# Kernel tuning notes

Hardware: AMD Instinct MI355X
Metric: run time of the kernel (lower is better)

## Reference

```python
import jax, jax.numpy as jnp
import numpy as np
import math

D = 1024      # hidden_size
H = 16        # num_heads
HD = D // H   # head_dim = 64
ROPE = 64     # rope_dim == head_dim (full-head rotation, empty pass-through)
E = 8         # num_experts
F = 2560
BASE = 10000.0
EPS = 1e-5
SPECIALS = jnp.arange(2, 8)  # special_tokens indices {2..7} used as global tokens


def _ln(x, w, b):
    m = x.mean(-1, keepdims=True)
    v = x.var(-1, keepdims=True)  # biased var, matches torch LayerNorm
    return (x - m) / jnp.sqrt(v + EPS) * w + b


def _rope(x, cos, sin):
    # x: [B,H,T,HD]; rotate first ROPE dims via half-split (NOT rotate-half interleave)
    x1, x2 = x[..., : ROPE // 2], x[..., ROPE // 2 : ROPE]
    rot = jnp.concatenate([x1 * cos - x2 * sin, x1 * sin + x2 * cos], axis=-1)
    return jnp.concatenate([rot, x[..., ROPE:]], axis=-1)


def setup_inputs() -> dict:
    key = jax.random.key(0)
    ks = jax.random.split(key, 8)
    B, T = 1, 1024
    g = lambda k, shape, s: (jax.random.normal(k, shape, jnp.float32) * s)
    return {
        "x": g(ks[0], (B, T, D), 1.0),
        "input_ids": jax.random.randint(ks[1], (B, T), 0, 32000),
        "ln1_w": jnp.ones((D,), jnp.float32), "ln1_b": jnp.zeros((D,), jnp.float32),
        "qkv_w": g(ks[2], (D, 3 * D), 0.02), "qkv_b": jnp.zeros((3 * D,), jnp.float32),
        "attn_out_w": g(ks[3], (D, D), 0.02), "attn_out_b": jnp.zeros((D,), jnp.float32),
        "ln2_w": jnp.ones((D,), jnp.float32), "ln2_b": jnp.zeros((D,), jnp.float32),
        "gate_w": g(ks[4], (D, E), 0.02), "gate_b": jnp.zeros((E,), jnp.float32),
        "fc_w": g(ks[5], (E, D, 2 * F), 0.02), "fc_b": jnp.zeros((E, 2 * F), jnp.float32),
        "eout_w": g(ks[6], (E, F, D), 0.02), "eout_b": jnp.zeros((E, D), jnp.float32),
    }


def _block(x, input_ids, ln1_w, ln1_b, qkv_w, qkv_b, attn_out_w, attn_out_b,
           ln2_w, ln2_b, gate_w, gate_b, fc_w, fc_b, eout_w, eout_b):
    B, T, _ = x.shape
    # --- self-attention (pre-norm) ---
    h = _ln(x, ln1_w, ln1_b)
    qkv = h @ qkv_w + qkv_b
    q, k, v = jnp.split(qkv, 3, axis=-1)
    resh = lambda t: t.reshape(B, T, H, HD).transpose(0, 2, 1, 3)  # [B,H,T,HD]
    q, k, v = resh(q), resh(k), resh(v)
    pos = jnp.arange(T, dtype=jnp.float32)
    inv = 1.0 / (BASE ** (jnp.arange(0, ROPE, 2, dtype=jnp.float32) / ROPE))
    fr = pos[:, None] * inv[None, :]            # [T, ROPE/2]
    cos, sin = jnp.cos(fr), jnp.sin(fr)
    q = _rope(q, cos, sin)
    k = _rope(k, cos, sin)
    causal = jnp.tril(jnp.ones((T, T), bool))
    glob = (input_ids[..., None] == SPECIALS).any(-1)            # [B,T]
    allowed = causal[None, None] | glob[:, None, :, None]        # [B,1,T,T]
    logits = jnp.einsum('bhqd,bhkd->bhqk', q, k) / math.sqrt(HD)
    neg = -jnp.finfo(logits.dtype).max
    logits = jnp.where(allowed, logits, neg)
    aw = jax.nn.softmax(logits, axis=-1)
    attn = jnp.einsum('bhqk,bhkd->bhqd', aw, v).transpose(0, 2, 1, 3).reshape(B, T, H * HD)
    x = x + (attn @ attn_out_w + attn_out_b)
    # --- MoE GEGLU FFN (hard top-1 routing) ---
    h2 = _ln(x, ln2_w, ln2_b)
    gp = jax.nn.softmax(h2 @ gate_w + gate_b, axis=-1)           # [B,T,E]
    gw = gp.max(-1)
    gi = gp.argmax(-1)
    xf = h2.reshape(-1, D)
    gif = gi.reshape(-1)
    gwf = gw.reshape(-1)
    N = xf.shape[0]
    outf = jnp.zeros((N, D), x.dtype)
    for e in range(E):  # fixed small expert loop; select by routing mask
        h12 = xf @ fc_w[e] + fc_b[e]
        x1, x2 = h12[:, :F], h12[:, F:]
        y = (x1 * jax.nn.gelu(x2, approximate=False)) @ eout_w[e] + eout_b[e]
        outf = outf + jnp.where((gif == e)[:, None], y, 0.0)
    outf = outf * gwf[:, None]
    sums = jax.ops.segment_sum(gwf, gif, num_segments=E)
    counts = jax.ops.segment_sum(jnp.ones_like(gwf), gif, num_segments=E)
    usage = sums / (counts + 1e-8)
    moe_loss = jnp.sum((usage - 1.0 / E) ** 2)
    return x + outf.reshape(B, T, D), moe_loss


def reference(x, input_ids, ln1_w, ln1_b, qkv_w, qkv_b, attn_out_w, attn_out_b,
              ln2_w, ln2_b, gate_w, gate_b, fc_w, fc_b, eout_w, eout_b):
    return _block(x, input_ids, ln1_w, ln1_b, qkv_w, qkv_b, attn_out_w, attn_out_b,
                  ln2_w, ln2_b, gate_w, gate_b, fc_w, fc_b, eout_w, eout_b)
```

## Files before the change

kernel.cpp:

```cpp
#include <hip/hip_runtime.h>
#include <float.h>
#include <math.h>
#include <stdint.h>

#define T_ 1024
#define D_ 1024
#define H_ 16
#define HD_ 64
#define E_ 8
#define F_ 2560
#define D3_ 3072
#define F2_ 5120

#define WS_H    0u
#define WS_QKV  1048576u
#define WS_ATTN 4194304u
#define WS_X2   5242880u
#define WS_H2   6291456u
#define WS_A    7340032u
#define WS_GW   9961472u
#define WS_GI   9962496u
#define WS_OFFS 9963520u
#define WS_PERM 9963536u

typedef short short8 __attribute__((ext_vector_type(8)));
typedef short short4v __attribute__((ext_vector_type(4)));
typedef __bf16 bf16x8 __attribute__((ext_vector_type(8)));
typedef float floatx4 __attribute__((ext_vector_type(4)));

union FragU { short8 s; bf16x8 b; };

__device__ __forceinline__ short f2bf(float f) {
    union { float f; uint32_t u; } a; a.f = f;
    uint32_t r = a.u + 0x7fffu + ((a.u >> 16) & 1u);
    return (short)(r >> 16);
}

__device__ __forceinline__ void cvt16(const float4& a0, const float4& a1,
                                      const float4& a2, const float4& a3,
                                      short8& c0, short8& c1) {
    c0[0]=f2bf(a0.x); c0[1]=f2bf(a0.y); c0[2]=f2bf(a0.z); c0[3]=f2bf(a0.w);
    c0[4]=f2bf(a1.x); c0[5]=f2bf(a1.y); c0[6]=f2bf(a1.z); c0[7]=f2bf(a1.w);
    c1[0]=f2bf(a2.x); c1[1]=f2bf(a2.y); c1[2]=f2bf(a2.z); c1[3]=f2bf(a2.w);
    c1[4]=f2bf(a3.x); c1[5]=f2bf(a3.y); c1[6]=f2bf(a3.z); c1[7]=f2bf(a3.w);
}

#define GEMM_IDS \
    const int tid  = threadIdx.x;                 \
    const int a_m  = tid >> 1;                    \
    const int a_kh = (tid & 1) * 16;              \
    const int lane = tid & 63, wave = tid >> 6;   \
    const int wm = wave & 1,  wn = wave >> 1;     \
    const int quad = lane >> 4, lm = lane & 15;

__global__ __launch_bounds__(256) void gemm_mfma_full(
    const float* __restrict__ A, int lda,
    const float* __restrict__ B, int ldb,
    const float* __restrict__ bias,
    float* __restrict__ C, int ldc, int K)
{
    __shared__ __align__(16) short As[4*128*8];
    __shared__ __align__(16) short Bs[64*40];
    const int row0 = blockIdx.y * 128, col0 = blockIdx.x * 64;
    GEMM_IDS
    const int b_n = tid >> 2, b_kc = tid & 3;
    floatx4 acc[4][2];
    #pragma unroll
    for (int i=0;i<4;i++)
        #pragma unroll
        for (int j=0;j<2;j++) acc[i][j] = (floatx4){0.f,0.f,0.f,0.f};

    const float* apx = A + (size_t)(row0 + a_m) * lda + a_kh;
    const float* bpx = B + (size_t)(b_kc*8) * ldb + col0 + b_n;
    const int kcA = (tid & 1) * 2;

    float4 a0, a1, a2, a3; float bvv[8];
    a0 = *(const float4*)(apx);     a1 = *(const float4*)(apx + 4);
    a2 = *(const float4*)(apx + 8); a3 = *(const float4*)(apx + 12);
    #pragma unroll
    for (int j=0;j<8;j++) bvv[j] = bpx[(size_t)j*ldb];

    for (int k0 = 0; k0 < K; k0 += 32) {
        __syncthreads();
        short8 c0, c1, cb;
        cvt16(a0,a1,a2,a3,c0,c1);
        #pragma unroll
        for (int j=0;j<8;j++) cb[j] = f2bf(bvv[j]);
        *(short8*)&As[((kcA  )*128 + a_m)*8] = c0;
        *(short8*)&As[((kcA+1)*128 + a_m)*8] = c1;
        *(short8*)&Bs[b_n*40 + b_kc*8] = cb;
        __syncthreads();
        if (k0 + 32 < K) {
            const float* ap2 = apx + k0 + 32;
            a0 = *(const float4*)(ap2);     a1 = *(const float4*)(ap2 + 4);
            a2 = *(const float4*)(ap2 + 8); a3 = *(const float4*)(ap2 + 12);
            const float* bp2 = bpx + (size_t)(k0+32) * ldb;
            #pragma unroll
            for (int j=0;j<8;j++) bvv[j] = bp2[(size_t)j*ldb];
        }
        FragU fa[4], fb[2];
        #pragma unroll
        for (int i=0;i<4;i++) fa[i].s = *(short8*)&As[(quad*128 + wm*64 + i*16 + lm)*8];
        #pragma unroll
        for (int j=0;j<2;j++) fb[j].s = *(short8*)&Bs[(wn*32 + j*16 + lm)*40 + quad*8];
        #pragma unroll
        for (int i=0;i<4;i++)
            #pragma unroll
            for (int j=0;j<2;j++)
                acc[i][j] = __builtin_amdgcn_mfma_f32_16x16x32_bf16(fa[i].b, fb[j].b, acc[i][j], 0,0,0);
    }
    #pragma unroll
    for (int i=0;i<4;i++)
        #pragma unroll
        for (int j=0;j<2;j++) {
            int col = col0 + wn*32 + j*16 + lm;
            float bb = bias ? bias[col] : 0.f;
            #pragma unroll
            for (int r=0;r<4;r++) {
                int row = row0 + wm*64 + i*16 + quad*4 + r;
                C[(size_t)row*ldc + col] = acc[i][j][r] + bb;
            }
        }
}

__global__ __launch_bounds__(256) void gemm_mfma_acc(
    const float* __restrict__ A, int lda,
    const float* __restrict__ B, int ldb, long sB,
    const int* __restrict__ offs, const int* __restrict__ perm,
    float* __restrict__ Cacc, int ldc, int K, int nsk)
{
    const int sk = blockIdx.z % nsk;
    const int e  = blockIdx.z / nsk;
    int off = 0, Ne = T_;
    if (offs) { off = offs[e]; Ne = offs[e+1] - off; }
    const int row0 = blockIdx.y * 128;
    if (row0 >= Ne) return;
    const int col0 = blockIdx.x * 64;
    B += (long)e * sB;

    __shared__ __align__(16) short As[4*128*8];
    __shared__ __align__(16) short Bs[64*40];
    __shared__ int toks[128];
    GEMM_IDS
    const int b_n = tid >> 2, b_kc = tid & 3;
    if (tid < 128) {
        int r = row0 + tid;
        toks[tid] = offs ? ((r < Ne) ? perm[off + r] : -1) : r;
    }
    __syncthreads();

    floatx4 acc[4][2];
    #pragma unroll
    for (int i=0;i<4;i++)
        #pragma unroll
        for (int j=0;j<2;j++) acc[i][j] = (floatx4){0.f,0.f,0.f,0.f};

    const int tokA = toks[a_m];
    const float* apx = (tokA >= 0) ? (A + (size_t)tokA * lda + a_kh) : nullptr;
    const float* bpx = B + (size_t)(b_kc*8) * ldb + col0 + b_n;
    const int kcA = (tid & 1) * 2;
    const int Kp = K / nsk;
    const int koff = sk * Kp, kend = koff + Kp;

    float4 a0, a1, a2, a3; float bvv[8];
    a0 = make_float4(0,0,0,0); a1 = a0; a2 = a0; a3 = a0;
    if (apx) {
        a0 = *(const float4*)(apx + koff);     a1 = *(const float4*)(apx + koff + 4);
        a2 = *(const float4*)(apx + koff + 8); a3 = *(const float4*)(apx + koff + 12);
    }
    {
        const float* bp2 = bpx + (size_t)koff * ldb;
        #pragma unroll
        for (int j=0;j<8;j++) bvv[j] = bp2[(size_t)j*ldb];
    }

    for (int k0 = koff; k0 < kend; k0 += 32) {
        __syncthreads();
        short8 c0, c1, cb;
        cvt16(a0,a1,a2,a3,c0,c1);
        #pragma unroll
        for (int j=0;j<8;j++) cb[j] = f2bf(bvv[j]);
        *(short8*)&As[((kcA  )*128 + a_m)*8] = c0;
        *(short8*)&As[((kcA+1)*128 + a_m)*8] = c1;
        *(short8*)&Bs[b_n*40 + b_kc*8] = cb;
        __syncthreads();
        if (k0 + 32 < kend) {
            if (apx) {
                const float* ap2 = apx + k0 + 32;
                a0 = *(const float4*)(ap2);     a1 = *(const float4*)(ap2 + 4);
                a2 = *(const float4*)(ap2 + 8); a3 = *(const float4*)(ap2 + 12);
            }
            const float* bp2 = bpx + (size_t)(k0+32) * ldb;
            #pragma unroll
            for (int j=0;j<8;j++) bvv[j] = bp2[(size_t)j*ldb];
        }
        FragU fa[4], fb[2];
        #pragma unroll
        for (int i=0;i<4;i++) fa[i].s = *(short8*)&As[(quad*128 + wm*64 + i*16 + lm)*8];
        #pragma unroll
        for (int j=0;j<2;j++) fb[j].s = *(short8*)&Bs[(wn*32 + j*16 + lm)*40 + quad*8];
        #pragma unroll
        for (int i=0;i<4;i++)
            #pragma unroll
            for (int j=0;j<2;j++)
                acc[i][j] = __builtin_amdgcn_mfma_f32_16x16x32_bf16(fa[i].b, fb[j].b, acc[i][j], 0,0,0);
    }
    #pragma unroll
    for (int i=0;i<4;i++)
        #pragma unroll
        for (int j=0;j<2;j++) {
            int col = col0 + wn*32 + j*16 + lm;
            #pragma unroll
            for (int r=0;r<4;r++) {
                int tk = toks[wm*64 + i*16 + quad*4 + r];
                if (tk >= 0) atomicAdd(&Cacc[(size_t)tk*ldc + col], acc[i][j][r]);
            }
        }
}

__global__ __launch_bounds__(256) void moe_fc_mfma(
    const float* __restrict__ h2, const float* __restrict__ fcw,
    const float* __restrict__ fcb, const int* __restrict__ offs,
    const int* __restrict__ perm, float* __restrict__ aout)
{
    const int e = blockIdx.z;
    const int off = offs[e];
    const int Ne = offs[e+1] - off;
    const int row0 = blockIdx.y * 128;
    if (row0 >= Ne) return;
    const int col0 = blockIdx.x * 32;

    __shared__ __align__(16) short As[4*128*8];
    __shared__ __align__(16) short B1s[32*40];
    __shared__ __align__(16) short B2s[32*40];
    __shared__ int toks[128];
    GEMM_IDS
    const int n_l = tid & 31, kg = tid >> 5;
    if (tid < 128) {
        int r = row0 + tid;
        toks[tid] = (r < Ne) ? perm[off + r] : -1;
    }
    __syncthreads();

    floatx4 acc1[4], acc2[4];
    #pragma unroll
    for (int i=0;i<4;i++) {
        acc1[i] = (floatx4){0.f,0.f,0.f,0.f};
        acc2[i] = (floatx4){0.f,0.f,0.f,0.f};
    }

    const float* W = fcw + (size_t)e * D_ * F2_;
    const int tokA = toks[a_m];
    const float* apx = (tokA >= 0) ? (h2 + (size_t)tokA * D_ + a_kh) : nullptr;
    const float* bpx = W + (size_t)(kg*4) * F2_ + col0 + n_l;
    const int kcA = (tid & 1) * 2;

    float4 a0, a1, a2, a3; float b1v[4], b2v[4];
    a0 = make_float4(0,0,0,0); a1 = a0; a2 = a0; a3 = a0;
    if (apx) {
        a0 = *(const float4*)(apx);     a1 = *(const float4*)(apx + 4);
        a2 = *(const float4*)(apx + 8); a3 = *(const float4*)(apx + 12);
    }
    #pragma unroll
    for (int j=0;j<4;j++) { b1v[j] = bpx[(size_t)j*F2_]; b2v[j] = bpx[(size_t)j*F2_ + F_]; }

    for (int k0 = 0; k0 < D_; k0 += 32) {
        __syncthreads();
        short8 c0, c1;
        short4v cb1, cb2;
        cvt16(a0,a1,a2,a3,c0,c1);
        #pragma unroll
        for (int j=0;j<4;j++) { cb1[j] = f2bf(b1v[j]); cb2[j] = f2bf(b2v[j]); }
        *(short8*)&As[((kcA  )*128 + a_m)*8] = c0;
        *(short8*)&As[((kcA+1)*128 + a_m)*8] = c1;
        *(short4v*)&B1s[n_l*40 + kg*4] = cb1;
        *(short4v*)&B2s[n_l*40 + kg*4] = cb2;
        __syncthreads();
        if (k0 + 32 < D_) {
            if (apx) {
                const float* ap2 = apx + k0 + 32;
                a0 = *(const float4*)(ap2);     a1 = *(const float4*)(ap2 + 4);
                a2 = *(const float4*)(ap2 + 8); a3 = *(const float4*)(ap2 + 12);
            }
            const float* bp2 = bpx + (size_t)(k0+32) * F2_;
            #pragma unroll
            for (int j=0;j<4;j++) { b1v[j] = bp2[(size_t)j*F2_]; b2v[j] = bp2[(size_t)j*F2_ + F_]; }
        }
        FragU fa[4], fb1, fb2;
        #pragma unroll
        for (int i=0;i<4;i++) fa[i].s = *(short8*)&As[(quad*128 + wm*64 + i*16 + lm)*8];
        fb1.s = *(short8*)&B1s[(wn*16 + lm)*40 + quad*8];
        fb2.s = *(short8*)&B2s[(wn*16 + lm)*40 + quad*8];
        #pragma unroll
        for (int i=0;i<4;i++) {
            acc1[i] = __builtin_amdgcn_mfma_f32_16x16x32_bf16(fa[i].b, fb1.b, acc1[i], 0,0,0);
            acc2[i] = __builtin_amdgcn_mfma_f32_16x16x32_bf16(fa[i].b, fb2.b, acc2[i], 0,0,0);
        }
    }
    {
        int col = col0 + wn*16 + lm;
        float b1 = fcb[(size_t)e*F2_ + col];
        float b2 = fcb[(size_t)e*F2_ + F_ + col];
        #pragma unroll
        for (int i=0;i<4;i++)
            #pragma unroll
            for (int r=0;r<4;r++) {
                int tk = toks[wm*64 + i*16 + quad*4 + r];
                if (tk < 0) continue;
                float v1 = acc1[i][r] + b1;
                float v2 = acc2[i][r] + b2;
                float g = v2 * 0.5f * (1.0f + erff(v2 * 0.70710678118654752f));
                aout[(size_t)tk*F_ + col] = v1 * g;
            }
    }
}

__global__ __launch_bounds__(128) void flash_attn(
    const float* __restrict__ qkv, const int* __restrict__ ids,
    float* __restrict__ attnout)
{
    const int h  = blockIdx.y;
    const int q0 = blockIdx.x * 32;
    const int tid = threadIdx.x;
    const int lane = tid & 63, w = tid >> 6;
    const int quad = lane >> 4, lm = lane & 15;

    __shared__ __align__(16) short Qs[32*72];
    __shared__ __align__(16) short Ks[64*72];
    __shared__ __align__(16) short Vt[64*72];
    __shared__ __align__(16) short Ps[2][16*72];
    __shared__ int globf[32];

    {
        int row = tid >> 2, c = (tid & 3) * 16;
        const float* qp = qkv + (size_t)(q0 + row) * D3_ + h * HD_ + c;
        float4 f0 = *(const float4*)(qp);
        float4 f1 = *(const float4*)(qp + 4);
        float4 f2 = *(const float4*)(qp + 8);
        float4 f3 = *(const float4*)(qp + 12);
        short8 s0, s1;
        cvt16(f0, f1, f2, f3, s0, s1);
        *(short8*)&Qs[row*72 + c]     = s0;
        *(short8*)&Qs[row*72 + c + 8] = s1;
    }
    if (tid < 32) {
        int id = ids[q0 + tid];
        globf[tid] = (id >= 2 && id <= 7) ? 1 : 0;
    }
    __syncthreads();

    FragU QA[2];
    #pragma unroll
    for (int s = 0; s < 2; s++)
        QA[s].s = *(short8*)&Qs[(w*16 + lm)*72 + s*32 + quad*8];

    int any = 0;
    #pragma unroll
    for (int i = 0; i < 32; i++) any |= globf[i];
    const int nt = any ? (T_/64) : ((q0 + 31) >> 6) + 1;

    int gq[4]; int qidx[4];
    #pragma unroll
    for (int r = 0; r < 4; r++) {
        int ql = w*16 + quad*4 + r;
        qidx[r] = q0 + ql;
        gq[r] = globf[ql];
    }

    float mrow[4] = {-1e30f, -1e30f, -1e30f, -1e30f};
    float lrow[4] = {0.f, 0.f, 0.f, 0.f};
    floatx4 Oacc[4];
    #pragma unroll
    for (int n = 0; n < 4; n++) Oacc[n] = (floatx4){0.f, 0.f, 0.f, 0.f};

    for (int kt = 0; kt < nt; kt++) {
        __syncthreads();
        #pragma unroll
        for (int rep = 0; rep < 2; rep++) {
            int key = (tid >> 2) + rep*32;
            int c = (tid & 3) * 16;
            const float* kp = qkv + (size_t)(kt*64 + key) * D3_ + D_ + h*HD_ + c;
            float4 f0 = *(const float4*)(kp);
            float4 f1 = *(const float4*)(kp + 4);
            float4 f2 = *(const float4*)(kp + 8);
            float4 f3 = *(const float4*)(kp + 12);
            short8 s0, s1;
            cvt16(f0, f1, f2, f3, s0, s1);
            *(short8*)&Ks[key*72 + c]     = s0;
            *(short8*)&Ks[key*72 + c + 8] = s1;
        }
        #pragma unroll
        for (int rep = 0; rep < 8; rep++) {
            int lin = tid + rep*128;
            int key = lin >> 4;
            int c = (lin & 15) * 4;
            const float* vp = qkv + (size_t)(kt*64 + key) * D3_ + 2*D_ + h*HD_ + c;
            float4 f = *(const float4*)vp;
            Vt[(c+0)*72 + key] = f2bf(f.x);
            Vt[(c+1)*72 + key] = f2bf(f.y);
            Vt[(c+2)*72 + key] = f2bf(f.z);
            Vt[(c+3)*72 + key] = f2bf(f.w);
        }
        __syncthreads();

        floatx4 Sv[4];
        #pragma unroll
        for (int n = 0; n < 4; n++) {
            Sv[n] = (floatx4){0.f, 0.f, 0.f, 0.f};
            #pragma unroll
            for (int s = 0; s < 2; s++) {
                FragU KB;
                KB.s = *(short8*)&Ks[(n*16 + lm)*72 + s*32 + quad*8];
                Sv[n] = __builtin_amdgcn_mfma_f32_16x16x32_bf16(QA[s].b, KB.b, Sv[n], 0, 0, 0);
            }
        }
        #pragma unroll
        for (int n = 0; n < 4; n++) {
            int key = kt*64 + n*16 + lm;
            #pragma unroll
            for (int r = 0; r < 4; r++) {
                float v = Sv[n][r] * 0.125f;
                if (!gq[r] && key > qidx[r]) v = -1e30f;
                Sv[n][r] = v;
            }
        }
        float mnew[4], alpha[4], tsum[4];
        #pragma unroll
        for (int r = 0; r < 4; r++) {
            float tm = fmaxf(fmaxf(Sv[0][r], Sv[1][r]), fmaxf(Sv[2][r], Sv[3][r]));
            #pragma unroll
            for (int x = 1; x < 16; x <<= 1) tm = fmaxf(tm, __shfl_xor(tm, x));
            mnew[r] = fmaxf(mrow[r], tm);
            alpha[r] = __expf(mrow[r] - mnew[r]);
            mrow[r] = mnew[r];
            tsum[r] = 0.f;
        }
        #pragma unroll
        for (int n = 0; n < 4; n++) {
            #pragma unroll
            for (int r = 0; r < 4; r++) {
                float p = __expf(Sv[n][r] - mnew[r]);
                tsum[r] += p;
                Ps[w][(quad*4 + r)*72 + n*16 + lm] = f2bf(p);
            }
        }
        #pragma unroll
        for (int r = 0; r < 4; r++) {
            #pragma unroll
            for (int x = 1; x < 16; x <<= 1) tsum[r] += __shfl_xor(tsum[r], x);
            lrow[r] = lrow[r] * alpha[r] + tsum[r];
        }
        #pragma unroll
        for (int n = 0; n < 4; n++)
            #pragma unroll
            for (int r = 0; r < 4; r++) Oacc[n][r] *= alpha[r];

        #pragma unroll
        for (int s = 0; s < 2; s++) {
            FragU PA;
            PA.s = *(short8*)&Ps[w][lm*72 + s*32 + quad*8];
            #pragma unroll
            for (int n = 0; n < 4; n++) {
                FragU VB;
                VB.s = *(short8*)&Vt[(n*16 + lm)*72 + s*32 + quad*8];
                Oacc[n] = __builtin_amdgcn_mfma_f32_16x16x32_bf16(PA.b, VB.b, Oacc[n], 0, 0, 0);
            }
        }
    }

    #pragma unroll
    for (int n = 0; n < 4; n++)
        #pragma unroll
        for (int r = 0; r < 4; r++) {
            float o = Oacc[n][r] / lrow[r];
            attnout[(size_t)qidx[r]*D_ + h*HD_ + n*16 + lm] = o;
        }
}

__global__ __launch_bounds__(256) void ep_attn(
    const float* __restrict__ x, const float* __restrict__ sacc,
    const float* __restrict__ aob, float* __restrict__ x2)
{
    int row = blockIdx.x, tid = threadIdx.x;
    float4 xv = ((const float4*)(x + (size_t)row*D_))[tid];
    float4 sv = ((const float4*)(sacc + (size_t)row*D_))[tid];
    float4 bv = ((const float4*)aob)[tid];
    float4 o;
    o.x = xv.x + sv.x + bv.x; o.y = xv.y + sv.y + bv.y;
    o.z = xv.z + sv.z + bv.z; o.w = xv.w + sv.w + bv.w;
    ((float4*)(x2 + (size_t)row*D_))[tid] = o;
}

__global__ __launch_bounds__(256) void ep_moe(
    const float* __restrict__ x2, const float* __restrict__ sacc,
    const float* __restrict__ eob, const float* __restrict__ gw,
    const int* __restrict__ gi, float* __restrict__ out)
{
    int row = blockIdx.x, tid = threadIdx.x;
    float g = gw[row];
    int e = gi[row];
    float4 xv = ((const float4*)(x2 + (size_t)row*D_))[tid];
    float4 sv = ((const float4*)(sacc + (size_t)row*D_))[tid];
    float4 bv = ((const float4*)(eob + (size_t)e*D_))[tid];
    float4 o;
    o.x = xv.x + g*(sv.x + bv.x); o.y = xv.y + g*(sv.y + bv.y);
    o.z = xv.z + g*(sv.z + bv.z); o.w = xv.w + g*(sv.w + bv.w);
    ((float4*)(out + (size_t)row*D_))[tid] = o;
}

__global__ __launch_bounds__(256) void ln_kernel(
    const float* __restrict__ x, const float* __restrict__ w,
    const float* __restrict__ b, float* __restrict__ out)
{
    const int row = blockIdx.x, tid = threadIdx.x;
    const int lane = tid & 63, wave = tid >> 6;
    float4 v = ((const float4*)(x + (size_t)row * D_))[tid];
    float s  = v.x + v.y + v.z + v.w;
    float sq = v.x*v.x + v.y*v.y + v.z*v.z + v.w*v.w;
    #pragma unroll
    for (int off = 32; off; off >>= 1) {
        s  += __shfl_down(s, off);
        sq += __shfl_down(sq, off);
    }
    __shared__ float rs[4], rq[4], mv[2];
    if (lane == 0) { rs[wave] = s; rq[wave] = sq; }
    __syncthreads();
    if (tid == 0) {
        float ts = rs[0]+rs[1]+rs[2]+rs[3];
        float tq = rq[0]+rq[1]+rq[2]+rq[3];
        float mean = ts * (1.0f / D_);
        float var  = tq * (1.0f / D_) - mean*mean;
        mv[0] = mean; mv[1] = rsqrtf(var + 1e-5f);
    }
    __syncthreads();
    float mean = mv[0], rstd = mv[1];
    float4 wv = ((const float4*)w)[tid];
    float4 bv = ((const float4*)b)[tid];
    float4 o;
    o.x = (v.x-mean)*rstd*wv.x + bv.x;
    o.y = (v.y-mean)*rstd*wv.y + bv.y;
    o.z = (v.z-mean)*rstd*wv.z + bv.z;
    o.w = (v.w-mean)*rstd*wv.w + bv.w;
    ((float4*)(out + (size_t)row * D_))[tid] = o;
}

__global__ __launch_bounds__(256) void rope_kernel(float* __restrict__ qkv)
{
    int gid = blockIdx.x * 256 + threadIdx.x;
    int t = gid >> 9;
    int r = gid & 511;
    int h = r >> 5;
    int d = r & 31;
    float inv = exp2f((float)d * -0.4152410118609203f);
    float fr = (float)t * inv;
    float s, c;
    sincosf(fr, &s, &c);
    float* base = qkv + (size_t)t*D3_ + h*HD_ + d;
    float q1 = base[0], q2 = base[32];
    base[0]  = q1*c - q2*s;
    base[32] = q1*s + q2*c;
    float* kb = base + D_;
    float k1 = kb[0], k2 = kb[32];
    kb[0]  = k1*c - k2*s;
    kb[32] = k1*s + k2*c;
}

__global__ __launch_bounds__(256) void ln2_gate_kernel(
    const float* __restrict__ x2, const float* __restrict__ w,
    const float* __restrict__ b, const float* __restrict__ gwm,
    const float* __restrict__ gbv, float* __restrict__ h2,
    int* __restrict__ gi, float* __restrict__ gw)
{
    const int row = blockIdx.x, tid = threadIdx.x;
    const int lane = tid & 63, wave = tid >> 6;
    float4 v = ((const float4*)(x2 + (size_t)row * D_))[tid];
    float s  = v.x + v.y + v.z + v.w;
    float sq = v.x*v.x + v.y*v.y + v.z*v.z + v.w*v.w;
    #pragma unroll
    for (int off = 32; off; off >>= 1) {
        s  += __shfl_down(s, off);
        sq += __shfl_down(sq, off);
    }
    __shared__ float rs[4], rq[4], mv[2];
    if (lane == 0) { rs[wave] = s; rq[wave] = sq; }
    __syncthreads();
    if (tid == 0) {
        float ts = rs[0]+rs[1]+rs[2]+rs[3];
        float tq = rq[0]+rq[1]+rq[2]+rq[3];
        float mean = ts * (1.0f / D_);
        float var  = tq * (1.0f / D_) - mean*mean;
        mv[0] = mean; mv[1] = rsqrtf(var + 1e-5f);
    }
    __syncthreads();
    float mean = mv[0], rstd = mv[1];
    float4 wv = ((const float4*)w)[tid];
    float4 bv = ((const float4*)b)[tid];
    float hv[4];
    hv[0] = (v.x-mean)*rstd*wv.x + bv.x;
    hv[1] = (v.y-mean)*rstd*wv.y + bv.y;
    hv[2] = (v.z-mean)*rstd*wv.z + bv.z;
    hv[3] = (v.w-mean)*rstd*wv.w + bv.w;
    float4 o; o.x=hv[0]; o.y=hv[1]; o.z=hv[2]; o.w=hv[3];
    ((float4*)(h2 + (size_t)row * D_))[tid] = o;

    float acc[E_] = {};
    int c = tid * 4;
    #pragma unroll
    for (int j = 0; j < 4; j++) {
        const float* gr = gwm + (size_t)(c+j) * E_;
        #pragma unroll
        for (int e = 0; e < E_; e++) acc[e] += hv[j] * gr[e];
    }
    #pragma unroll
    for (int off = 32; off; off >>= 1)
        #pragma unroll
        for (int e = 0; e < E_; e++) acc[e] += __shfl_down(acc[e], off);
    __shared__ float gred[4][E_];
    if (lane == 0)
        for (int e = 0; e < E_; e++) gred[wave][e] = acc[e];
    __syncthreads();
    if (tid == 0) {
        float lg[E_];
        float mxl = -FLT_MAX; int mi = 0;
        for (int e = 0; e < E_; e++)
            lg[e] = gred[0][e]+gred[1][e]+gred[2][e]+gred[3][e] + gbv[e];
        for (int e = 0; e < E_; e++)
            if (lg[e] > mxl) { mxl = lg[e]; mi = e; }
        float ssum = 0.f;
        for (int e = 0; e < E_; e++) ssum += expf(lg[e] - mxl);
        gi[row] = mi;
        gw[row] = 1.0f / ssum;
    }
}

__global__ void route_kernel(const int* __restrict__ gi,
                             int* __restrict__ offs, int* __restrict__ perm)
{
    __shared__ int cnt[E_], c2[E_], off[E_+1];
    const int tid = threadIdx.x;
    if (tid < E_) { cnt[tid] = 0; c2[tid] = 0; }
    __syncthreads();
    int e = gi[tid];
    atomicAdd(&cnt[e], 1);
    __syncthreads();
    if (tid == 0) {
        off[0] = 0;
        for (int i = 0; i < E_; i++) off[i+1] = off[i] + cnt[i];
        for (int i = 0; i <= E_; i++) offs[i] = off[i];
    }
    __syncthreads();
    int r = atomicAdd(&c2[e], 1);
    perm[off[e] + r] = tid;
}

__global__ void loss_kernel(const int* __restrict__ gi,
                            const float* __restrict__ gw, float* __restrict__ out)
{
    __shared__ float ss[E_], sc[E_];
    const int tid = threadIdx.x;
    if (tid < E_) { ss[tid] = 0.f; sc[tid] = 0.f; }
    __syncthreads();
    for (int t = tid; t < T_; t += 256) {
        int e = gi[t];
        atomicAdd(&ss[e], gw[t]);
        atomicAdd(&sc[e], 1.0f);
    }
    __syncthreads();
    if (tid == 0) {
        float loss = 0.f;
        for (int e = 0; e < E_; e++) {
            float u = ss[e] / (sc[e] + 1e-8f);
            float d = u - 0.125f;
            loss += d * d;
        }
        out[(size_t)T_ * D_] = loss;
    }
}

extern "C" void kernel_launch(void* const* d_in, const int* in_sizes, int n_in,
                              void* d_out, int out_size, void* d_ws, size_t ws_size,
                              hipStream_t stream)
{
    const float* x     = (const float*)d_in[0];
    const int*   ids   = (const int*)d_in[1];
    const float* ln1w  = (const float*)d_in[2];
    const float* ln1b  = (const float*)d_in[3];
    const float* qkvw  = (const float*)d_in[4];
    const float* qkvb  = (const float*)d_in[5];
    const float* aow   = (const float*)d_in[6];
    const float* aob   = (const float*)d_in[7];
    const float* ln2w  = (const float*)d_in[8];
    const float* ln2b  = (const float*)d_in[9];
    const float* gatew = (const float*)d_in[10];
    const float* gateb = (const float*)d_in[11];
    const float* fcw   = (const float*)d_in[12];
    const float* fcb   = (const float*)d_in[13];
    const float* eoutw = (const float*)d_in[14];
    const float* eoutb = (const float*)d_in[15];
    float* out = (float*)d_out;
    float* ws  = (float*)d_ws;

    float* h    = ws + WS_H;
    float* sacc = ws + WS_H;
    float* qkv  = ws + WS_QKV;
    float* attn = ws + WS_ATTN;
    float* x2   = ws + WS_X2;
    float* h2   = ws + WS_H2;
    float* abuf = ws + WS_A;
    float* gw   = ws + WS_GW;
    int*   gi   = (int*)(ws + WS_GI);
    int*   offs = (int*)(ws + WS_OFFS);
    int*   perm = (int*)(ws + WS_PERM);

    ln_kernel<<<T_, 256, 0, stream>>>(x, ln1w, ln1b, h);
    gemm_mfma_full<<<dim3(D3_/64, T_/128), 256, 0, stream>>>(
        h, D_, qkvw, D3_, qkvb, qkv, D3_, D_);
    rope_kernel<<<(T_*H_*32)/256, 256, 0, stream>>>(qkv);
    flash_attn<<<dim3(T_/32, H_), 128, 0, stream>>>(qkv, ids, attn);
    hipMemsetAsync(sacc, 0, (size_t)T_*D_*sizeof(float), stream);
    gemm_mfma_acc<<<dim3(D_/64, T_/128, 4), 256, 0, stream>>>(
        attn, D_, aow, D_, 0, nullptr, nullptr, sacc, D_, D_, 4);
    ep_attn<<<T_, 256, 0, stream>>>(x, sacc, aob, x2);
    ln2_gate_kernel<<<T_, 256, 0, stream>>>(x2, ln2w, ln2b, gatew, gateb, h2, gi, gw);
    route_kernel<<<1, T_, 0, stream>>>(gi, offs, perm);
    moe_fc_mfma<<<dim3(F_/32, T_/128, E_), 256, 0, stream>>>(h2, fcw, fcb, offs, perm, abuf);
    hipMemsetAsync(sacc, 0, (size_t)T_*D_*sizeof(float), stream);
    gemm_mfma_acc<<<dim3(D_/64, T_/128, 4*E_), 256, 0, stream>>>(
        abuf, F_, eoutw, D_, (long)F_*D_, offs, perm, sacc, D_, F_, 4);
    ep_moe<<<T_, 256, 0, stream>>>(x2, sacc, eoutb, gw, gi, out);
    loss_kernel<<<1, 256, 0, stream>>>(gi, gw, out);
}
```

Baseline: 589.8 us.

## Store GEMM A-operand activations as bf16 and double-buffer global prefetch

Producer kernels (LN1, LN2, flash attention, MoE fc) now write their outputs as bf16 instead of fp32. The downstream GEMMs then load the A operand directly as short8, which halves activation traffic and removes the per-tile conversion. The GEMM k-loops are unrolled by two with two register prefetch buffers, so global loads are issued further ahead of their use. Grid dimensions are also reordered so the expert/split-k index is on y and the row tile on z, which changes block scheduling order. Numerics are unchanged in practice because the MFMA already consumed bf16, but register pressure rises with the extra prefetch buffers.

```diff
diff --git a/kernel.cpp b/kernel.cpp
--- a/kernel.cpp
+++ b/kernel.cpp
@@ -54,7 +54,7 @@
     const int quad = lane >> 4, lm = lane & 15;
 
 __global__ __launch_bounds__(256) void gemm_mfma_full(
-    const float* __restrict__ A, int lda,
+    const short* __restrict__ A, int lda,
     const float* __restrict__ B, int ldb,
     const float* __restrict__ bias,
     float* __restrict__ C, int ldc, int K)
@@ -70,45 +70,61 @@
         #pragma unroll
         for (int j=0;j<2;j++) acc[i][j] = (floatx4){0.f,0.f,0.f,0.f};
 
-    const float* apx = A + (size_t)(row0 + a_m) * lda + a_kh;
+    const short* apx = A + (size_t)(row0 + a_m) * lda + a_kh;
     const float* bpx = B + (size_t)(b_kc*8) * ldb + col0 + b_n;
     const int kcA = (tid & 1) * 2;
 
-    float4 a0, a1, a2, a3; float bvv[8];
-    a0 = *(const float4*)(apx);     a1 = *(const float4*)(apx + 4);
-    a2 = *(const float4*)(apx + 8); a3 = *(const float4*)(apx + 12);
-    #pragma unroll
-    for (int j=0;j<8;j++) bvv[j] = bpx[(size_t)j*ldb];
-
-    for (int k0 = 0; k0 < K; k0 += 32) {
-        __syncthreads();
-        short8 c0, c1, cb;
-        cvt16(a0,a1,a2,a3,c0,c1);
-        #pragma unroll
-        for (int j=0;j<8;j++) cb[j] = f2bf(bvv[j]);
-        *(short8*)&As[((kcA  )*128 + a_m)*8] = c0;
-        *(short8*)&As[((kcA+1)*128 + a_m)*8] = c1;
-        *(short8*)&Bs[b_n*40 + b_kc*8] = cb;
-        __syncthreads();
-        if (k0 + 32 < K) {
-            const float* ap2 = apx + k0 + 32;
-            a0 = *(const float4*)(ap2);     a1 = *(const float4*)(ap2 + 4);
-            a2 = *(const float4*)(ap2 + 8); a3 = *(const float4*)(ap2 + 12);
-            const float* bp2 = bpx + (size_t)(k0+32) * ldb;
-            #pragma unroll
-            for (int j=0;j<8;j++) bvv[j] = bp2[(size_t)j*ldb];
-        }
-        FragU fa[4], fb[2];
-        #pragma unroll
-        for (int i=0;i<4;i++) fa[i].s = *(short8*)&As[(quad*128 + wm*64 + i*16 + lm)*8];
-        #pragma unroll
-        for (int j=0;j<2;j++) fb[j].s = *(short8*)&Bs[(wn*32 + j*16 + lm)*40 + quad*8];
-        #pragma unroll
-        for (int i=0;i<4;i++)
-            #pragma unroll
-            for (int j=0;j<2;j++)
-                acc[i][j] = __builtin_amdgcn_mfma_f32_16x16x32_bf16(fa[i].b, fb[j].b, acc[i][j], 0,0,0);
-    }
+    short8 sA0, sA1, sB0, sB1;
+    float bvA[8], bvB[8];
+    sA0 = *(const short8*)(apx);
+    sA1 = *(const short8*)(apx + 8);
+    sB0 = *(const short8*)(apx + 32);
+    sB1 = *(const short8*)(apx + 40);
+    #pragma unroll
+    for (int j=0;j<8;j++) bvA[j] = bpx[(size_t)j*ldb];
+    {
+        const float* bp2 = bpx + (size_t)32*ldb;
+        #pragma unroll
+        for (int j=0;j<8;j++) bvB[j] = bp2[(size_t)j*ldb];
+    }
+
+#define GF_STEP(S0,S1,BV,kpre)                                            \
+    __syncthreads();                                                      \
+    {                                                                     \
+        short8 cb;                                                        \
+        _Pragma("unroll")                                                 \
+        for (int j=0;j<8;j++) cb[j] = f2bf(BV[j]);                        \
+        *(short8*)&As[((kcA  )*128 + a_m)*8] = S0;                        \
+        *(short8*)&As[((kcA+1)*128 + a_m)*8] = S1;                        \
+        *(short8*)&Bs[b_n*40 + b_kc*8] = cb;                              \
+    }                                                                     \
+    __syncthreads();                                                      \
+    if ((kpre) < K) {                                                     \
+        S0 = *(const short8*)(apx + (kpre));                              \
+        S1 = *(const short8*)(apx + (kpre) + 8);                          \
+        const float* bp2 = bpx + (size_t)(kpre) * ldb;                    \
+        _Pragma("unroll")                                                 \
+        for (int j=0;j<8;j++) BV[j] = bp2[(size_t)j*ldb];                 \
+    }                                                                     \
+    {                                                                     \
+        FragU fa[4], fb[2];                                               \
+        _Pragma("unroll")                                                 \
+        for (int i=0;i<4;i++) fa[i].s = *(short8*)&As[(quad*128 + wm*64 + i*16 + lm)*8]; \
+        _Pragma("unroll")                                                 \
+        for (int j=0;j<2;j++) fb[j].s = *(short8*)&Bs[(wn*32 + j*16 + lm)*40 + quad*8];  \
+        _Pragma("unroll")                                                 \
+        for (int i=0;i<4;i++)                                             \
+            _Pragma("unroll")                                             \
+            for (int j=0;j<2;j++)                                         \
+                acc[i][j] = __builtin_amdgcn_mfma_f32_16x16x32_bf16(fa[i].b, fb[j].b, acc[i][j], 0,0,0); \
+    }
+
+    for (int k0 = 0; k0 < K; k0 += 64) {
+        GF_STEP(sA0, sA1, bvA, k0 + 64)
+        GF_STEP(sB0, sB1, bvB, k0 + 96)
+    }
+#undef GF_STEP
+
     #pragma unroll
     for (int i=0;i<4;i++)
         #pragma unroll
@@ -124,16 +140,16 @@
 }
 
 __global__ __launch_bounds__(256) void gemm_mfma_acc(
-    const float* __restrict__ A, int lda,
+    const short* __restrict__ A, int lda,
     const float* __restrict__ B, int ldb, long sB,
     const int* __restrict__ offs, const int* __restrict__ perm,
     float* __restrict__ Cacc, int ldc, int K, int nsk)
 {
-    const int sk = blockIdx.z % nsk;
-    const int e  = blockIdx.z / nsk;
+    const int sk = blockIdx.y % nsk;
+    const int e  = blockIdx.y / nsk;
     int off = 0, Ne = T_;
     if (offs) { off = offs[e]; Ne = offs[e+1] - off; }
-    const int row0 = blockIdx.y * 128;
+    const int row0 = blockIdx.z * 128;
     if (row0 >= Ne) return;
     const int col0 = blockIdx.x * 64;
     B += (long)e * sB;
@@ -156,55 +172,68 @@
         for (int j=0;j<2;j++) acc[i][j] = (floatx4){0.f,0.f,0.f,0.f};
 
     const int tokA = toks[a_m];
-    const float* apx = (tokA >= 0) ? (A + (size_t)tokA * lda + a_kh) : nullptr;
+    const short* apx = (tokA >= 0) ? (A + (size_t)tokA * lda + a_kh) : nullptr;
     const float* bpx = B + (size_t)(b_kc*8) * ldb + col0 + b_n;
     const int kcA = (tid & 1) * 2;
     const int Kp = K / nsk;
     const int koff = sk * Kp, kend = koff + Kp;
 
-    float4 a0, a1, a2, a3; float bvv[8];
-    a0 = make_float4(0,0,0,0); a1 = a0; a2 = a0; a3 = a0;
+    short8 sA0 = {0,0,0,0,0,0,0,0}, sA1 = sA0, sB0 = sA0, sB1 = sA0;
+    float bvA[8], bvB[8];
     if (apx) {
-        a0 = *(const float4*)(apx + koff);     a1 = *(const float4*)(apx + koff + 4);
-        a2 = *(const float4*)(apx + koff + 8); a3 = *(const float4*)(apx + koff + 12);
+        sA0 = *(const short8*)(apx + koff);
+        sA1 = *(const short8*)(apx + koff + 8);
+        sB0 = *(const short8*)(apx + koff + 32);
+        sB1 = *(const short8*)(apx + koff + 40);
     }
     {
         const float* bp2 = bpx + (size_t)koff * ldb;
         #pragma unroll
-        for (int j=0;j<8;j++) bvv[j] = bp2[(size_t)j*ldb];
-    }
-
-    for (int k0 = koff; k0 < kend; k0 += 32) {
-        __syncthreads();
-        short8 c0, c1, cb;
-        cvt16(a0,a1,a2,a3,c0,c1);
-        #pragma unroll
-        for (int j=0;j<8;j++) cb[j] = f2bf(bvv[j]);
-        *(short8*)&As[((kcA  )*128 + a_m)*8] = c0;
-        *(short8*)&As[((kcA+1)*128 + a_m)*8] = c1;
-        *(short8*)&Bs[b_n*40 + b_kc*8] = cb;
-        __syncthreads();
-        if (k0 + 32 < kend) {
-            if (apx) {
-                const float* ap2 = apx + k0 + 32;
-                a0 = *(const float4*)(ap2);     a1 = *(const float4*)(ap2 + 4);
-                a2 = *(const float4*)(ap2 + 8); a3 = *(const float4*)(ap2 + 12);
-            }
-            const float* bp2 = bpx + (size_t)(k0+32) * ldb;
-            #pragma unroll
-            for (int j=0;j<8;j++) bvv[j] = bp2[(size_t)j*ldb];
-        }
-        FragU fa[4], fb[2];
-        #pragma unroll
-        for (int i=0;i<4;i++) fa[i].s = *(short8*)&As[(quad*128 + wm*64 + i*16 + lm)*8];
-        #pragma unroll
-        for (int j=0;j<2;j++) fb[j].s = *(short8*)&Bs[(wn*32 + j*16 + lm)*40 + quad*8];
-        #pragma unroll
-        for (int i=0;i<4;i++)
-            #pragma unroll
-            for (int j=0;j<2;j++)
-                acc[i][j] = __builtin_amdgcn_mfma_f32_16x16x32_bf16(fa[i].b, fb[j].b, acc[i][j], 0,0,0);
-    }
+        for (int j=0;j<8;j++) bvA[j] = bp2[(size_t)j*ldb];
+        bp2 += (size_t)32 * ldb;
+        #pragma unroll
+        for (int j=0;j<8;j++) bvB[j] = bp2[(size_t)j*ldb];
+    }
+
+#define GA_STEP(S0,S1,BV,kpre)                                            \
+    __syncthreads();                                                      \
+    {                                                                     \
+        short8 cb;                                                        \
+        _Pragma("unroll")                                                 \
+        for (int j=0;j<8;j++) cb[j] = f2bf(BV[j]);                        \
+        *(short8*)&As[((kcA  )*128 + a_m)*8] = S0;                        \
+        *(short8*)&As[((kcA+1)*128 + a_m)*8] = S1;                        \
+        *(short8*)&Bs[b_n*40 + b_kc*8] = cb;                              \
+    }                                                                     \
+    __syncthreads();                                                      \
+    if ((kpre) < kend) {                                                  \
+        if (apx) {                                                        \
+            S0 = *(const short8*)(apx + (kpre));                          \
+            S1 = *(const short8*)(apx + (kpre) + 8);                      \
+        }                                                                 \
+        const float* bp2 = bpx + (size_t)(kpre) * ldb;                    \
+        _Pragma("unroll")                                                 \
+        for (int j=0;j<8;j++) BV[j] = bp2[(size_t)j*ldb];                 \
+    }                                                                     \
+    {                                                                     \
+        FragU fa[4], fb[2];                                               \
+        _Pragma("unroll")                                                 \
+        for (int i=0;i<4;i++) fa[i].s = *(short8*)&As[(quad*128 + wm*64 + i*16 + lm)*8]; \
+        _Pragma("unroll")                                                 \
+        for (int j=0;j<2;j++) fb[j].s = *(short8*)&Bs[(wn*32 + j*16 + lm)*40 + quad*8];  \
+        _Pragma("unroll")                                                 \
+        for (int i=0;i<4;i++)                                             \
+            _Pragma("unroll")                                             \
+            for (int j=0;j<2;j++)                                         \
+                acc[i][j] = __builtin_amdgcn_mfma_f32_16x16x32_bf16(fa[i].b, fb[j].b, acc[i][j], 0,0,0); \
+    }
+
+    for (int k0 = koff; k0 < kend; k0 += 64) {
+        GA_STEP(sA0, sA1, bvA, k0 + 64)
+        GA_STEP(sB0, sB1, bvB, k0 + 96)
+    }
+#undef GA_STEP
+
     #pragma unroll
     for (int i=0;i<4;i++)
         #pragma unroll
@@ -219,14 +248,14 @@
 }
 
 __global__ __launch_bounds__(256) void moe_fc_mfma(
-    const float* __restrict__ h2, const float* __restrict__ fcw,
+    const short* __restrict__ h2, const float* __restrict__ fcw,
     const float* __restrict__ fcb, const int* __restrict__ offs,
-    const int* __restrict__ perm, float* __restrict__ aout)
-{
-    const int e = blockIdx.z;
+    const int* __restrict__ perm, short* __restrict__ aout)
+{
+    const int e = blockIdx.y;
     const int off = offs[e];
     const int Ne = offs[e+1] - off;
-    const int row0 = blockIdx.y * 128;
+    const int row0 = blockIdx.z * 128;
     if (row0 >= Ne) return;
     const int col0 = blockIdx.x * 32;
 
@@ -251,52 +280,66 @@
 
     const float* W = fcw + (size_t)e * D_ * F2_;
     const int tokA = toks[a_m];
-    const float* apx = (tokA >= 0) ? (h2 + (size_t)tokA * D_ + a_kh) : nullptr;
+    const short* apx = (tokA >= 0) ? (h2 + (size_t)tokA * D_ + a_kh) : nullptr;
     const float* bpx = W + (size_t)(kg*4) * F2_ + col0 + n_l;
     const int kcA = (tid & 1) * 2;
 
-    float4 a0, a1, a2, a3; float b1v[4], b2v[4];
-    a0 = make_float4(0,0,0,0); a1 = a0; a2 = a0; a3 = a0;
+    short8 sA0 = {0,0,0,0,0,0,0,0}, sA1 = sA0, sB0 = sA0, sB1 = sA0;
+    float b1A[4], b2A[4], b1B[4], b2B[4];
     if (apx) {
-        a0 = *(const float4*)(apx);     a1 = *(const float4*)(apx + 4);
-        a2 = *(const float4*)(apx + 8); a3 = *(const float4*)(apx + 12);
-    }
-    #pragma unroll
-    for (int j=0;j<4;j++) { b1v[j] = bpx[(size_t)j*F2_]; b2v[j] = bpx[(size_t)j*F2_ + F_]; }
-
-    for (int k0 = 0; k0 < D_; k0 += 32) {
-        __syncthreads();
-        short8 c0, c1;
-        short4v cb1, cb2;
-        cvt16(a0,a1,a2,a3,c0,c1);
-        #pragma unroll
-        for (int j=0;j<4;j++) { cb1[j] = f2bf(b1v[j]); cb2[j] = f2bf(b2v[j]); }
-        *(short8*)&As[((kcA  )*128 + a_m)*8] = c0;
-        *(short8*)&As[((kcA+1)*128 + a_m)*8] = c1;
-        *(short4v*)&B1s[n_l*40 + kg*4] = cb1;
-        *(short4v*)&B2s[n_l*40 + kg*4] = cb2;
-        __syncthreads();
-        if (k0 + 32 < D_) {
-            if (apx) {
-                const float* ap2 = apx + k0 + 32;
-                a0 = *(const float4*)(ap2);     a1 = *(const float4*)(ap2 + 4);
-                a2 = *(const float4*)(ap2 + 8); a3 = *(const float4*)(ap2 + 12);
-            }
-            const float* bp2 = bpx + (size_t)(k0+32) * F2_;
-            #pragma unroll
-            for (int j=0;j<4;j++) { b1v[j] = bp2[(size_t)j*F2_]; b2v[j] = bp2[(size_t)j*F2_ + F_]; }
-        }
-        FragU fa[4], fb1, fb2;
-        #pragma unroll
-        for (int i=0;i<4;i++) fa[i].s = *(short8*)&As[(quad*128 + wm*64 + i*16 + lm)*8];
-        fb1.s = *(short8*)&B1s[(wn*16 + lm)*40 + quad*8];
-        fb2.s = *(short8*)&B2s[(wn*16 + lm)*40 + quad*8];
-        #pragma unroll
-        for (int i=0;i<4;i++) {
-            acc1[i] = __builtin_amdgcn_mfma_f32_16x16x32_bf16(fa[i].b, fb1.b, acc1[i], 0,0,0);
-            acc2[i] = __builtin_amdgcn_mfma_f32_16x16x32_bf16(fa[i].b, fb2.b, acc2[i], 0,0,0);
-        }
-    }
+        sA0 = *(const short8*)(apx);
+        sA1 = *(const short8*)(apx + 8);
+        sB0 = *(const short8*)(apx + 32);
+        sB1 = *(const short8*)(apx + 40);
+    }
+    #pragma unroll
+    for (int j=0;j<4;j++) { b1A[j] = bpx[(size_t)j*F2_]; b2A[j] = bpx[(size_t)j*F2_ + F_]; }
+    {
+        const float* bp2 = bpx + (size_t)32*F2_;
+        #pragma unroll
+        for (int j=0;j<4;j++) { b1B[j] = bp2[(size_t)j*F2_]; b2B[j] = bp2[(size_t)j*F2_ + F_]; }
+    }
+
+#define MF_STEP(S0,S1,BV1,BV2,kpre)                                       \
+    __syncthreads();                                                      \
+    {                                                                     \
+        short4v cb1, cb2;                                                 \
+        _Pragma("unroll")                                                 \
+        for (int j=0;j<4;j++) { cb1[j] = f2bf(BV1[j]); cb2[j] = f2bf(BV2[j]); } \
+        *(short8*)&As[((kcA  )*128 + a_m)*8] = S0;                        \
+        *(short8*)&As[((kcA+1)*128 + a_m)*8] = S1;                        \
+        *(short4v*)&B1s[n_l*40 + kg*4] = cb1;                             \
+        *(short4v*)&B2s[n_l*40 + kg*4] = cb2;                             \
+    }                                                                     \
+    __syncthreads();                                                      \
+    if ((kpre) < D_) {                                                    \
+        if (apx) {                                                        \
+            S0 = *(const short8*)(apx + (kpre));                          \
+            S1 = *(const short8*)(apx + (kpre) + 8);                      \
+        }                                                                 \
+        const float* bp2 = bpx + (size_t)(kpre) * F2_;                    \
+        _Pragma("unroll")                                                 \
+        for (int j=0;j<4;j++) { BV1[j] = bp2[(size_t)j*F2_]; BV2[j] = bp2[(size_t)j*F2_ + F_]; } \
+    }                                                                     \
+    {                                                                     \
+        FragU fa[4], fb1, fb2;                                            \
+        _Pragma("unroll")                                                 \
+        for (int i=0;i<4;i++) fa[i].s = *(short8*)&As[(quad*128 + wm*64 + i*16 + lm)*8]; \
+        fb1.s = *(short8*)&B1s[(wn*16 + lm)*40 + quad*8];                 \
+        fb2.s = *(short8*)&B2s[(wn*16 + lm)*40 + quad*8];                 \
+        _Pragma("unroll")                                                 \
+        for (int i=0;i<4;i++) {                                           \
+            acc1[i] = __builtin_amdgcn_mfma_f32_16x16x32_bf16(fa[i].b, fb1.b, acc1[i], 0,0,0); \
+            acc2[i] = __builtin_amdgcn_mfma_f32_16x16x32_bf16(fa[i].b, fb2.b, acc2[i], 0,0,0); \
+        }                                                                 \
+    }
+
+    for (int k0 = 0; k0 < D_; k0 += 64) {
+        MF_STEP(sA0, sA1, b1A, b2A, k0 + 64)
+        MF_STEP(sB0, sB1, b1B, b2B, k0 + 96)
+    }
+#undef MF_STEP
+
     {
         int col = col0 + wn*16 + lm;
         float b1 = fcb[(size_t)e*F2_ + col];
@@ -310,14 +353,14 @@
                 float v1 = acc1[i][r] + b1;
                 float v2 = acc2[i][r] + b2;
                 float g = v2 * 0.5f * (1.0f + erff(v2 * 0.70710678118654752f));
-                aout[(size_t)tk*F_ + col] = v1 * g;
+                aout[(size_t)tk*F_ + col] = f2bf(v1 * g);
             }
     }
 }
 
 __global__ __launch_bounds__(128) void flash_attn(
     const float* __restrict__ qkv, const int* __restrict__ ids,
-    float* __restrict__ attnout)
+    short* __restrict__ attnout)
 {
     const int h  = blockIdx.y;
     const int q0 = blockIdx.x * 32;
@@ -473,7 +516,7 @@
         #pragma unroll
         for (int r = 0; r < 4; r++) {
             float o = Oacc[n][r] / lrow[r];
-            attnout[(size_t)qidx[r]*D_ + h*HD_ + n*16 + lm] = o;
+            attnout[(size_t)qidx[r]*D_ + h*HD_ + n*16 + lm] = f2bf(o);
         }
 }
 
@@ -510,7 +553,7 @@
 
 __global__ __launch_bounds__(256) void ln_kernel(
     const float* __restrict__ x, const float* __restrict__ w,
-    const float* __restrict__ b, float* __restrict__ out)
+    const float* __restrict__ b, short* __restrict__ out)
 {
     const int row = blockIdx.x, tid = threadIdx.x;
     const int lane = tid & 63, wave = tid >> 6;
@@ -536,12 +579,12 @@
     float mean = mv[0], rstd = mv[1];
     float4 wv = ((const float4*)w)[tid];
     float4 bv = ((const float4*)b)[tid];
-    float4 o;
-    o.x = (v.x-mean)*rstd*wv.x + bv.x;
-    o.y = (v.y-mean)*rstd*wv.y + bv.y;
-    o.z = (v.z-mean)*rstd*wv.z + bv.z;
-    o.w = (v.w-mean)*rstd*wv.w + bv.w;
-    ((float4*)(out + (size_t)row * D_))[tid] = o;
+    short4v o;
+    o[0] = f2bf((v.x-mean)*rstd*wv.x + bv.x);
+    o[1] = f2bf((v.y-mean)*rstd*wv.y + bv.y);
+    o[2] = f2bf((v.z-mean)*rstd*wv.z + bv.z);
+    o[3] = f2bf((v.w-mean)*rstd*wv.w + bv.w);
+    ((short4v*)(out + (size_t)row * D_))[tid] = o;
 }
 
 __global__ __launch_bounds__(256) void rope_kernel(float* __restrict__ qkv)
@@ -568,7 +611,7 @@
 __global__ __launch_bounds__(256) void ln2_gate_kernel(
     const float* __restrict__ x2, const float* __restrict__ w,
     const float* __restrict__ b, const float* __restrict__ gwm,
-    const float* __restrict__ gbv, float* __restrict__ h2,
+    const float* __restrict__ gbv, short* __restrict__ h2,
     int* __restrict__ gi, float* __restrict__ gw)
 {
     const int row = blockIdx.x, tid = threadIdx.x;
@@ -600,8 +643,9 @@
     hv[1] = (v.y-mean)*rstd*wv.y + bv.y;
     hv[2] = (v.z-mean)*rstd*wv.z + bv.z;
     hv[3] = (v.w-mean)*rstd*wv.w + bv.w;
-    float4 o; o.x=hv[0]; o.y=hv[1]; o.z=hv[2]; o.w=hv[3];
-    ((float4*)(h2 + (size_t)row * D_))[tid] = o;
+    short4v o;
+    o[0]=f2bf(hv[0]); o[1]=f2bf(hv[1]); o[2]=f2bf(hv[2]); o[3]=f2bf(hv[3]);
+    ((short4v*)(h2 + (size_t)row * D_))[tid] = o;
 
     float acc[E_] = {};
     int c = tid * 4;
@@ -700,32 +744,32 @@
     float* out = (float*)d_out;
     float* ws  = (float*)d_ws;
 
-    float* h    = ws + WS_H;
-    float* sacc = ws + WS_H;
-    float* qkv  = ws + WS_QKV;
-    float* attn = ws + WS_ATTN;
-    float* x2   = ws + WS_X2;
-    float* h2   = ws + WS_H2;
-    float* abuf = ws + WS_A;
-    float* gw   = ws + WS_GW;
-    int*   gi   = (int*)(ws + WS_GI);
-    int*   offs = (int*)(ws + WS_OFFS);
-    int*   perm = (int*)(ws + WS_PERM);
-
-    ln_kernel<<<T_, 256, 0, stream>>>(x, ln1w, ln1b, h);
+    short* hb    = (short*)(ws + WS_H);
+    float* sacc  = ws + WS_H;
+    float* qkv   = ws + WS_QKV;
+    short* attnb = (short*)(ws + WS_ATTN);
+    float* x2    = ws + WS_X2;
+    short* h2b   = (short*)(ws + WS_H2);
+    short* abuf  = (short*)(ws + WS_A);
+    float* gw    = ws + WS_GW;
+    int*   gi    = (int*)(ws + WS_GI);
+    int*   offs  = (int*)(ws + WS_OFFS);
+    int*   perm  = (int*)(ws + WS_PERM);
+
+    ln_kernel<<<T_, 256, 0, stream>>>(x, ln1w, ln1b, hb);
     gemm_mfma_full<<<dim3(D3_/64, T_/128), 256, 0, stream>>>(
-        h, D_, qkvw, D3_, qkvb, qkv, D3_, D_);
+        hb, D_, qkvw, D3_, qkvb, qkv, D3_, D_);
     rope_kernel<<<(T_*H_*32)/256, 256, 0, stream>>>(qkv);
-    flash_attn<<<dim3(T_/32, H_), 128, 0, stream>>>(qkv, ids, attn);
+    flash_attn<<<dim3(T_/32, H_), 128, 0, stream>>>(qkv, ids, attnb);
     hipMemsetAsync(sacc, 0, (size_t)T_*D_*sizeof(float), stream);
-    gemm_mfma_acc<<<dim3(D_/64, T_/128, 4), 256, 0, stream>>>(
-        attn, D_, aow, D_, 0, nullptr, nullptr, sacc, D_, D_, 4);
+    gemm_mfma_acc<<<dim3(D_/64, 4, T_/128), 256, 0, stream>>>(
+        attnb, D_, aow, D_, 0, nullptr, nullptr, sacc, D_, D_, 4);
     ep_attn<<<T_, 256, 0, stream>>>(x, sacc, aob, x2);
-    ln2_gate_kernel<<<T_, 256, 0, stream>>>(x2, ln2w, ln2b, gatew, gateb, h2, gi, gw);
+    ln2_gate_kernel<<<T_, 256, 0, stream>>>(x2, ln2w, ln2b, gatew, gateb, h2b, gi, gw);
     route_kernel<<<1, T_, 0, stream>>>(gi, offs, perm);
-    moe_fc_mfma<<<dim3(F_/32, T_/128, E_), 256, 0, stream>>>(h2, fcw, fcb, offs, perm, abuf);
+    moe_fc_mfma<<<dim3(F_/32, E_, T_/128), 256, 0, stream>>>(h2b, fcw, fcb, offs, perm, abuf);
     hipMemsetAsync(sacc, 0, (size_t)T_*D_*sizeof(float), stream);
-    gemm_mfma_acc<<<dim3(D_/64, T_/128, 4*E_), 256, 0, stream>>>(
+    gemm_mfma_acc<<<dim3(D_/64, 4*E_, T_/128), 256, 0, stream>>>(
         abuf, F_, eoutw, D_, (long)F_*D_, offs, perm, sacc, D_, F_, 4);
     ep_moe<<<T_, 256, 0, stream>>>(x2, sacc, eoutb, gw, gi, out);
     loss_kernel<<<1, 256, 0, stream>>>(gi, gw, out);
```

New measurement: 548.3 us. 7.0% less time.
